# Kernel tuning notes

Hardware: AMD Instinct MI355X
Metric: run time of the kernel (lower is better)

Reference implementation:

```python
import jax, jax.numpy as jnp
import numpy as np

B, N, C = 64, 1024, 128


def setup_inputs() -> dict:
    key = jax.random.key(0)
    k1, k2, k3, k4, k5, k6 = jax.random.split(key, 6)
    adj_vals = jax.random.uniform(k1, (B, N, N), dtype=jnp.float32)
    mask = jax.random.uniform(k2, (B, N, N)) < 0.1
    adjacent = jnp.where(mask, adj_vals, 0.0)
    annotations = jax.random.normal(k3, (B, N, C), dtype=jnp.float32)
    # GraphConvolution bias, shape (1,1,C)
    gc_bias = jax.random.normal(k4, (1, 1, C), dtype=jnp.float32) * 0.05
    # Keras GRU params (reset_after=True default): kernel (C,3C), recurrent (C,3C), bias (2,3C)
    kernel = jax.random.normal(k5, (C, 3 * C), dtype=jnp.float32) / np.sqrt(C)
    recurrent_kernel = jax.random.normal(k6, (C, 3 * C), dtype=jnp.float32) / np.sqrt(C)
    gru_bias = jnp.zeros((2, 3 * C), dtype=jnp.float32)
    return {"adjacent": adjacent, "annotations": annotations, "gc_bias": gc_bias,
            "kernel": kernel, "recurrent_kernel": recurrent_kernel, "gru_bias": gru_bias}


def reference(adjacent, annotations, gc_bias, kernel, recurrent_kernel, gru_bias):
    # GraphConvolution: per-graph adj @ annotations, batched, + bias
    v = jnp.einsum('bij,bjc->bic', adjacent, annotations) + gc_bias  # [B,N,C]
    b, n, c = v.shape
    x = v.reshape(-1, c)            # visible states, one GRU step each
    h = annotations.reshape(-1, c)  # initial hidden states
    # single-step Keras GRU (reset_after=True)
    mx = x @ kernel + gru_bias[0]
    mh = h @ recurrent_kernel + gru_bias[1]
    xz, xr, xh = jnp.split(mx, 3, axis=-1)
    hz, hr, hh_in = jnp.split(mh, 3, axis=-1)
    z = jax.nn.sigmoid(xz + hz)
    r = jax.nn.sigmoid(xr + hr)
    hh = jnp.tanh(xh + r * hh_in)
    out = z * h + (1.0 - z) * hh
    return out.reshape(b, n, c)
```

## Files before the change

kernel.cpp:

```cpp
#include <hip/hip_runtime.h>

typedef unsigned short ushort_t;
typedef __attribute__((ext_vector_type(8))) short bf16x8;
typedef __attribute__((ext_vector_type(8))) unsigned short u16x8;
typedef __attribute__((ext_vector_type(4))) float f32x4;

#define B_ 64
#define N_ 1024
#define C_ 128

static __device__ __forceinline__ unsigned short f2bf(float f) {
  union { float f; unsigned int i; } v; v.f = f;
  unsigned int i = v.i;
  return (unsigned short)((i + 0x7FFFu + ((i >> 16) & 1u)) >> 16);
}
static __device__ __forceinline__ void split1(float x, ushort_t& h, ushort_t& l) {
  union { float f; unsigned int i; } u; u.f = x;
  h = (ushort_t)(u.i >> 16);
  union { unsigned int i; float f; } t; t.i = u.i & 0xFFFF0000u;
  union { float f; unsigned int i; } w; w.f = x - t.f;
  l = (ushort_t)(w.i >> 16);
}
static __device__ __forceinline__ bf16x8 as_bf(u16x8 v) {
  union { u16x8 u; bf16x8 b; } x; x.u = v; return x.b;
}
static __device__ __forceinline__ void gload_lds16(const void* g, void* l) {
  __builtin_amdgcn_global_load_lds((const __attribute__((address_space(1))) void*)g,
                                   (__attribute__((address_space(3))) void*)l,
                                   16, 0, 0);
}

__global__ __launch_bounds__(256) void tsplit(const float* __restrict__ src,
                                              ushort_t* __restrict__ dh,
                                              ushort_t* __restrict__ dl,
                                              int rows, int cols, long sb, long db) {
  __shared__ float tile[64][65];
  const int t = threadIdx.x;
  src += (long)blockIdx.z * sb;
  dh  += (long)blockIdx.z * db;
  dl  += (long)blockIdx.z * db;
  const int r0 = blockIdx.y * 64, c0 = blockIdx.x * 64;
#pragma unroll
  for (int p = 0; p < 4; ++p) {
    int row = p * 16 + (t >> 4), c4 = (t & 15) * 4;
    f32x4 v = *(const f32x4*)(src + (long)(r0 + row) * cols + c0 + c4);
#pragma unroll
    for (int j = 0; j < 4; ++j) tile[row][c4 + j] = v[j];
  }
  __syncthreads();
  const int oc = t >> 2;
#pragma unroll
  for (int p = 0; p < 2; ++p) {
    int ck = (t & 3) + p * 4;
    u16x8 vh, vl;
#pragma unroll
    for (int j = 0; j < 8; ++j) {
      ushort_t hj, lj;
      split1(tile[ck * 8 + j][oc], hj, lj);
      vh[j] = hj; vl[j] = lj;
    }
    long o = (long)(c0 + oc) * rows + r0 + ck * 8;
    *(u16x8*)(dh + o) = vh;
    *(u16x8*)(dl + o) = vl;
  }
}

__global__ __launch_bounds__(256, 2) void gc_gemm(const float* __restrict__ adj,
                                                  const ushort_t* __restrict__ annTh,
                                                  const ushort_t* __restrict__ annTl,
                                                  const float* __restrict__ gcb,
                                                  float* __restrict__ vout) {
  __shared__ __align__(16) ushort_t ldsAh[128 * 64];
  __shared__ __align__(16) ushort_t ldsAl[128 * 64];
  __shared__ __align__(16) ushort_t ldsBh[128 * 64];
  __shared__ __align__(16) ushort_t ldsBl[128 * 64];
  const int tid = threadIdx.x;
  const int w = tid >> 6, lane = tid & 63;
  const int wr = w >> 1, wc = w & 1;
  const int swz = (blockIdx.x & 7) * 64 + (blockIdx.x >> 3);
  const int b = swz >> 3;
  const int m0 = (swz & 7) * 128;

  const float*    adjb = adj   + ((long)b * N_ + m0) * N_;
  const ushort_t* aThb = annTh + (long)b * C_ * N_;
  const ushort_t* aTlb = annTl + (long)b * C_ * N_;

  const int srow8 = lane >> 3;
  const int klog  = ((lane & 7) * 16) ^ (srow8 << 4);
  const int fr = lane & 15;
  const int kg = lane >> 4;

  f32x4 acc[4][4] = {};

  for (int k0 = 0; k0 < N_; k0 += 64) {
#pragma unroll
    for (int jj = 0; jj < 4; ++jj) {
      int j = w * 4 + jj;
      long so = (long)(j * 8 + srow8) * N_ + k0 + (klog >> 1);
      gload_lds16(aThb + so, (void*)&ldsBh[j * 512]);
      gload_lds16(aTlb + so, (void*)&ldsBl[j * 512]);
    }
#pragma unroll
    for (int q = 0; q < 4; ++q) {
      int ch = q * 256 + tid;
      int row = ch >> 3, ce = ch & 7;
      const float* g = adjb + (long)row * N_ + k0 + ce * 8;
      f32x4 a0 = *(const f32x4*)g;
      f32x4 a1 = *(const f32x4*)(g + 4);
      u16x8 vh, vl;
#pragma unroll
      for (int j = 0; j < 4; ++j) {
        ushort_t hj, lj;
        split1(a0[j], hj, lj); vh[j] = hj; vl[j] = lj;
        split1(a1[j], hj, lj); vh[4 + j] = hj; vl[4 + j] = lj;
      }
      int kb = (ce * 16) ^ ((row & 7) << 4);
      *(u16x8*)((char*)ldsAh + row * 128 + kb) = vh;
      *(u16x8*)((char*)ldsAl + row * 128 + kb) = vl;
    }
    __syncthreads();
#pragma unroll
    for (int kk = 0; kk < 2; ++kk) {
      bf16x8 ah[4], al[4], bh[4], bl[4];
#pragma unroll
      for (int mi = 0; mi < 4; ++mi) {
        int row = wr * 64 + mi * 16 + fr;
        int kb = (kk * 64 + kg * 16) ^ ((row & 7) << 4);
        ah[mi] = *(const bf16x8*)((const char*)ldsAh + row * 128 + kb);
        al[mi] = *(const bf16x8*)((const char*)ldsAl + row * 128 + kb);
      }
#pragma unroll
      for (int ni = 0; ni < 4; ++ni) {
        int row = wc * 64 + ni * 16 + fr;
        int kb = (kk * 64 + kg * 16) ^ ((row & 7) << 4);
        bh[ni] = *(const bf16x8*)((const char*)ldsBh + row * 128 + kb);
        bl[ni] = *(const bf16x8*)((const char*)ldsBl + row * 128 + kb);
      }
#pragma unroll
      for (int mi = 0; mi < 4; ++mi)
#pragma unroll
        for (int ni = 0; ni < 4; ++ni) {
          acc[mi][ni] = __builtin_amdgcn_mfma_f32_16x16x32_bf16(ah[mi], bh[ni], acc[mi][ni], 0, 0, 0);
          acc[mi][ni] = __builtin_amdgcn_mfma_f32_16x16x32_bf16(al[mi], bh[ni], acc[mi][ni], 0, 0, 0);
          acc[mi][ni] = __builtin_amdgcn_mfma_f32_16x16x32_bf16(ah[mi], bl[ni], acc[mi][ni], 0, 0, 0);
        }
    }
    __syncthreads();
  }

  const long rowbase = (long)b * N_ + m0 + wr * 64;
#pragma unroll
  for (int ni = 0; ni < 4; ++ni) {
    int col = wc * 64 + ni * 16 + fr;
    float bias = gcb[col];
#pragma unroll
    for (int mi = 0; mi < 4; ++mi)
#pragma unroll
      for (int r = 0; r < 4; ++r)
        vout[(rowbase + mi * 16 + kg * 4 + r) * C_ + col] = acc[mi][ni][r] + bias;
  }
}

__global__ __launch_bounds__(256, 2) void gru(const float* __restrict__ v,
                                              const float* __restrict__ ann,
                                              const ushort_t* __restrict__ kTh,
                                              const ushort_t* __restrict__ kTl,
                                              const ushort_t* __restrict__ rTh,
                                              const float* __restrict__ gb,
                                              float* __restrict__ out) {
  const int w = threadIdx.x >> 6, lane = threadIdx.x & 63;
  const long m0 = ((long)blockIdx.x * 4 + w) * 32;
  const int fr = lane & 15, kg = lane >> 4;

  bf16x8 xh[2][4], xl[2][4], hh[2][4];
#pragma unroll
  for (int s = 0; s < 2; ++s)
#pragma unroll
    for (int kk = 0; kk < 4; ++kk) {
      long off = (m0 + s * 16 + fr) * (long)C_ + kk * 32 + kg * 8;
      f32x4 x0 = *(const f32x4*)(v + off);
      f32x4 x1 = *(const f32x4*)(v + off + 4);
      u16x8 th, tl;
#pragma unroll
      for (int j = 0; j < 4; ++j) {
        ushort_t hj, lj;
        split1(x0[j], hj, lj); th[j] = hj; tl[j] = lj;
        split1(x1[j], hj, lj); th[4 + j] = hj; tl[4 + j] = lj;
      }
      xh[s][kk] = as_bf(th); xl[s][kk] = as_bf(tl);
      f32x4 h0 = *(const f32x4*)(ann + off);
      f32x4 h1 = *(const f32x4*)(ann + off + 4);
      u16x8 hv;
#pragma unroll
      for (int j = 0; j < 4; ++j) { hv[j] = f2bf(h0[j]); hv[4 + j] = f2bf(h1[j]); }
      hh[s][kk] = as_bf(hv);
    }

  bf16x8 W0K[4], W0L[4], W0R[4], W1K[4], W1L[4], W1R[4];
  float HV0[8], HV1[8];

#define LOADW(WK, WL, WR, NN, GG)                                              \
  {                                                                            \
    const ushort_t* kh_ = kTh + (long)((GG) * C_ + (NN) * 16 + fr) * C_;       \
    const ushort_t* kl_ = kTl + (long)((GG) * C_ + (NN) * 16 + fr) * C_;       \
    const ushort_t* rh_ = rTh + (long)((GG) * C_ + (NN) * 16 + fr) * C_;       \
    _Pragma("unroll")                                                          \
    for (int kk = 0; kk < 4; ++kk) {                                           \
      int o_ = kk * 32 + kg * 8;                                               \
      WK[kk] = *(const bf16x8*)(kh_ + o_);                                     \
      WL[kk] = *(const bf16x8*)(kl_ + o_);                                     \
      WR[kk] = *(const bf16x8*)(rh_ + o_);                                     \
    }                                                                          \
  }

#define LOADHV(HV, NN)                                                         \
  _Pragma("unroll")                                                            \
  for (int s = 0; s < 2; ++s)                                                  \
    _Pragma("unroll")                                                          \
    for (int r = 0; r < 4; ++r)                                                \
      HV[s * 4 + r] = ann[(m0 + s * 16 + kg * 4 + r) * (long)C_ + (NN) * 16 + fr];

#define MATH(WK, WL, WR, AK0, AK1, AR0, AR1)                                   \
  {                                                                            \
    _Pragma("unroll")                                                          \
    for (int kk = 0; kk < 4; ++kk) {                                           \
      AK0 = __builtin_amdgcn_mfma_f32_16x16x32_bf16(xh[0][kk], WK[kk], AK0, 0, 0, 0); \
      AK1 = __builtin_amdgcn_mfma_f32_16x16x32_bf16(xh[1][kk], WK[kk], AK1, 0, 0, 0); \
      AK0 = __builtin_amdgcn_mfma_f32_16x16x32_bf16(xl[0][kk], WK[kk], AK0, 0, 0, 0); \
      AK1 = __builtin_amdgcn_mfma_f32_16x16x32_bf16(xl[1][kk], WK[kk], AK1, 0, 0, 0); \
      AK0 = __builtin_amdgcn_mfma_f32_16x16x32_bf16(xh[0][kk], WL[kk], AK0, 0, 0, 0); \
      AK1 = __builtin_amdgcn_mfma_f32_16x16x32_bf16(xh[1][kk], WL[kk], AK1, 0, 0, 0); \
    }                                                                          \
    _Pragma("unroll")                                                          \
    for (int kk = 0; kk < 4; ++kk) {                                           \
      AR0 = __builtin_amdgcn_mfma_f32_16x16x32_bf16(hh[0][kk], WR[kk], AR0, 0, 0, 0); \
      AR1 = __builtin_amdgcn_mfma_f32_16x16x32_bf16(hh[1][kk], WR[kk], AR1, 0, 0, 0); \
    }                                                                          \
  }

#define EPILOGUE(NN, HV)                                                       \
  {                                                                            \
    const int cb = (NN) * 16 + fr;                                             \
    const float bz  = gb[cb] + gb[384 + cb];                                   \
    const float brr = gb[128 + cb] + gb[384 + 128 + cb];                       \
    const float bxh = gb[256 + cb];                                            \
    const float bhi = gb[384 + 256 + cb];                                      \
    _Pragma("unroll")                                                          \
    for (int s = 0; s < 2; ++s) {                                              \
      const f32x4& az_ = s ? az1 : az0;                                        \
      const f32x4& ar_ = s ? ar1 : ar0;                                        \
      const f32x4& ax_ = s ? ax1 : ax0;                                        \
      const f32x4& ah_ = s ? ah1 : ah0;                                        \
      _Pragma("unroll")                                                        \
      for (int r = 0; r < 4; ++r) {                                            \
        long row = m0 + s * 16 + kg * 4 + r;                                   \
        float hval = HV[s * 4 + r];                                            \
        float zz = 1.f / (1.f + __expf(-(az_[r] + bz)));                       \
        float rr = 1.f / (1.f + __expf(-(ar_[r] + brr)));                      \
        float hpre = ax_[r] + bxh + rr * (ah_[r] + bhi);                       \
        hpre = fminf(fmaxf(hpre, -15.f), 15.f);                                \
        float e2 = __expf(2.f * hpre);                                         \
        float th = (e2 - 1.f) / (e2 + 1.f);                                    \
        out[row * C_ + cb] = zz * hval + (1.f - zz) * th;                      \
      }                                                                        \
    }                                                                          \
  }

  LOADW(W0K, W0L, W0R, 0, 0)
  LOADHV(HV0, 0)

#pragma unroll 1
  for (int n = 0; n < 8; n += 2) {
    {
      f32x4 az0 = {}, az1 = {}, ar0 = {}, ar1 = {}, ax0 = {}, ax1 = {}, ah0 = {}, ah1 = {};
      LOADW(W1K, W1L, W1R, n, 1)
      MATH(W0K, W0L, W0R, az0, az1, az0, az1)
      LOADW(W0K, W0L, W0R, n, 2)
      MATH(W1K, W1L, W1R, ar0, ar1, ar0, ar1)
      LOADW(W1K, W1L, W1R, n + 1, 0)
      LOADHV(HV1, n + 1)
      MATH(W0K, W0L, W0R, ax0, ax1, ah0, ah1)
      EPILOGUE(n, HV0)
    }
    {
      f32x4 az0 = {}, az1 = {}, ar0 = {}, ar1 = {}, ax0 = {}, ax1 = {}, ah0 = {}, ah1 = {};
      LOADW(W0K, W0L, W0R, n + 1, 1)
      MATH(W1K, W1L, W1R, az0, az1, az0, az1)
      LOADW(W1K, W1L, W1R, n + 1, 2)
      MATH(W0K, W0L, W0R, ar0, ar1, ar0, ar1)
      const int nn2 = (n + 2 < 8) ? (n + 2) : 0;
      LOADW(W0K, W0L, W0R, nn2, 0)
      LOADHV(HV0, nn2)
      MATH(W1K, W1L, W1R, ax0, ax1, ah0, ah1)
      EPILOGUE(n + 1, HV1)
    }
  }
#undef LOADW
#undef LOADHV
#undef MATH
#undef EPILOGUE
}

extern "C" void kernel_launch(void* const* d_in, const int* in_sizes, int n_in,
                              void* d_out, int out_size, void* d_ws, size_t ws_size,
                              hipStream_t stream) {
  const float* adj = (const float*)d_in[0];
  const float* ann = (const float*)d_in[1];
  const float* gcb = (const float*)d_in[2];
  const float* ker = (const float*)d_in[3];
  const float* rk  = (const float*)d_in[4];
  const float* gb  = (const float*)d_in[5];
  float* out = (float*)d_out;

  char* ws = (char*)d_ws;
  ushort_t* annTh = (ushort_t*)(ws);
  ushort_t* annTl = (ushort_t*)(ws + 16777216);
  ushort_t* kTh   = (ushort_t*)(ws + 33554432);
  ushort_t* kTl   = (ushort_t*)(ws + 33652736);
  ushort_t* rTh   = (ushort_t*)(ws + 33751040);
  ushort_t* rTl   = (ushort_t*)(ws + 33849344);
  float*    vbuf  = (float*)(ws + 33947648);

  hipLaunchKernelGGL(tsplit, dim3(2, 16, 64), dim3(256), 0, stream,
                     ann, annTh, annTl, 1024, 128, (long)1024 * 128, (long)128 * 1024);
  hipLaunchKernelGGL(tsplit, dim3(6, 2, 1), dim3(256), 0, stream,
                     ker, kTh, kTl, 128, 384, 0L, 0L);
  hipLaunchKernelGGL(tsplit, dim3(6, 2, 1), dim3(256), 0, stream,
                     rk, rTh, rTl, 128, 384, 0L, 0L);
  hipLaunchKernelGGL(gc_gemm, dim3(512), dim3(256), 0, stream,
                     adj, annTh, annTl, gcb, vbuf);
  hipLaunchKernelGGL(gru, dim3(512), dim3(256), 0, stream,
                     vbuf, ann, kTh, kTl, rTh, gb, out);
}
```

Baseline: 203.6 us.

## Double-buffer gc_gemm with direct fp32 adjacency loads to LDS and in-register split

Reworks the adjacency GEMM main loop so the fp32 adjacency tile is copied straight into LDS with async global-to-LDS loads, instead of being loaded into registers, split into bf16 hi/lo and written to LDS. The bf16 split now happens after the LDS read, just before the MFMAs. LDS is double-buffered with a K-step of 32, so the next tile's loads are issued while the current tile is computed, with one barrier per iteration. The aim is to hide global memory latency and drop the register-staged conversion path. In exchange each wave repeats the split work in its compute phase and runs twice as many loop iterations.

```diff
diff --git a/kernel.cpp b/kernel.cpp
--- a/kernel.cpp
+++ b/kernel.cpp
@@ -70,10 +70,9 @@
                                                   const ushort_t* __restrict__ annTl,
                                                   const float* __restrict__ gcb,
                                                   float* __restrict__ vout) {
-  __shared__ __align__(16) ushort_t ldsAh[128 * 64];
-  __shared__ __align__(16) ushort_t ldsAl[128 * 64];
-  __shared__ __align__(16) ushort_t ldsBh[128 * 64];
-  __shared__ __align__(16) ushort_t ldsBl[128 * 64];
+  __shared__ __align__(16) float    ldsA [2 * 4096];
+  __shared__ __align__(16) ushort_t ldsBh[2 * 4096];
+  __shared__ __align__(16) ushort_t ldsBl[2 * 4096];
   const int tid = threadIdx.x;
   const int w = tid >> 6, lane = tid & 63;
   const int wr = w >> 1, wc = w & 1;
@@ -85,68 +84,84 @@
   const ushort_t* aThb = annTh + (long)b * C_ * N_;
   const ushort_t* aTlb = annTl + (long)b * C_ * N_;
 
-  const int srow8 = lane >> 3;
-  const int klog  = ((lane & 7) * 16) ^ (srow8 << 4);
   const int fr = lane & 15;
   const int kg = lane >> 4;
 
+  const int aRow  = lane >> 3;
+  const int aCs   = (lane & 7) ^ aRow;
+  const int bRow  = lane >> 2;
+  const int bCs   = (lane & 3) ^ ((lane >> 3) & 3);
+
   f32x4 acc[4][4] = {};
 
-  for (int k0 = 0; k0 < N_; k0 += 64) {
-#pragma unroll
-    for (int jj = 0; jj < 4; ++jj) {
-      int j = w * 4 + jj;
-      long so = (long)(j * 8 + srow8) * N_ + k0 + (klog >> 1);
-      gload_lds16(aThb + so, (void*)&ldsBh[j * 512]);
-      gload_lds16(aTlb + so, (void*)&ldsBl[j * 512]);
-    }
-#pragma unroll
-    for (int q = 0; q < 4; ++q) {
-      int ch = q * 256 + tid;
-      int row = ch >> 3, ce = ch & 7;
-      const float* g = adjb + (long)row * N_ + k0 + ce * 8;
-      f32x4 a0 = *(const f32x4*)g;
-      f32x4 a1 = *(const f32x4*)(g + 4);
-      u16x8 vh, vl;
-#pragma unroll
-      for (int j = 0; j < 4; ++j) {
-        ushort_t hj, lj;
-        split1(a0[j], hj, lj); vh[j] = hj; vl[j] = lj;
-        split1(a1[j], hj, lj); vh[4 + j] = hj; vl[4 + j] = lj;
-      }
-      int kb = (ce * 16) ^ ((row & 7) << 4);
-      *(u16x8*)((char*)ldsAh + row * 128 + kb) = vh;
-      *(u16x8*)((char*)ldsAl + row * 128 + kb) = vl;
-    }
+#define STAGE(CUR, T)                                                          \
+  {                                                                            \
+    const int k0_ = (T) * 32;                                                  \
+    _Pragma("unroll")                                                          \
+    for (int jj = 0; jj < 4; ++jj) {                                           \
+      int j_ = w * 4 + jj;                                                     \
+      gload_lds16(adjb + (long)(j_ * 8 + aRow) * N_ + k0_ + aCs * 4,           \
+                  (void*)(ldsA + (CUR) * 4096 + j_ * 256));                    \
+    }                                                                          \
+    _Pragma("unroll")                                                          \
+    for (int jj = 0; jj < 2; ++jj) {                                           \
+      int j_ = w * 2 + jj;                                                     \
+      long so_ = (long)(j_ * 16 + bRow) * N_ + k0_ + bCs * 8;                  \
+      gload_lds16(aThb + so_, (void*)(ldsBh + (CUR) * 4096 + j_ * 512));       \
+      gload_lds16(aTlb + so_, (void*)(ldsBl + (CUR) * 4096 + j_ * 512));       \
+    }                                                                          \
+  }
+
+#define COMPUTE(CUR)                                                           \
+  {                                                                            \
+    bf16x8 bh_[4], bl_[4], ah_[4], al_[4];                                     \
+    _Pragma("unroll")                                                          \
+    for (int ni = 0; ni < 4; ++ni) {                                           \
+      int row_ = wc * 64 + ni * 16 + fr;                                       \
+      int kb_ = (kg << 4) ^ ((((row_) >> 1) & 3) << 4);                        \
+      const char* base_ = (const char*)(ldsBh + (CUR) * 4096) + row_ * 64 + kb_; \
+      const char* basl_ = (const char*)(ldsBl + (CUR) * 4096) + row_ * 64 + kb_; \
+      bh_[ni] = *(const bf16x8*)base_;                                         \
+      bl_[ni] = *(const bf16x8*)basl_;                                         \
+    }                                                                          \
+    _Pragma("unroll")                                                          \
+    for (int mi = 0; mi < 4; ++mi) {                                           \
+      int row_ = wr * 64 + mi * 16 + fr;                                       \
+      int b0_ = row_ * 128 + ((kg * 32) ^ ((row_ & 7) << 4));                  \
+      f32x4 a0_ = *(const f32x4*)((const char*)(ldsA + (CUR) * 4096) + b0_);   \
+      f32x4 a1_ = *(const f32x4*)((const char*)(ldsA + (CUR) * 4096) + (b0_ ^ 16)); \
+      u16x8 vh_, vl_;                                                          \
+      _Pragma("unroll")                                                        \
+      for (int j = 0; j < 4; ++j) {                                            \
+        ushort_t hj_, lj_;                                                     \
+        split1(a0_[j], hj_, lj_); vh_[j] = hj_;     vl_[j] = lj_;              \
+        split1(a1_[j], hj_, lj_); vh_[4 + j] = hj_; vl_[4 + j] = lj_;          \
+      }                                                                        \
+      ah_[mi] = as_bf(vh_); al_[mi] = as_bf(vl_);                              \
+    }                                                                          \
+    _Pragma("unroll")                                                          \
+    for (int mi = 0; mi < 4; ++mi)                                             \
+      _Pragma("unroll")                                                        \
+      for (int ni = 0; ni < 4; ++ni) {                                         \
+        acc[mi][ni] = __builtin_amdgcn_mfma_f32_16x16x32_bf16(ah_[mi], bh_[ni], acc[mi][ni], 0, 0, 0); \
+        acc[mi][ni] = __builtin_amdgcn_mfma_f32_16x16x32_bf16(al_[mi], bh_[ni], acc[mi][ni], 0, 0, 0); \
+        acc[mi][ni] = __builtin_amdgcn_mfma_f32_16x16x32_bf16(ah_[mi], bl_[ni], acc[mi][ni], 0, 0, 0); \
+      }                                                                        \
+  }
+
+  STAGE(0, 0)
+  __syncthreads();
+
+#pragma unroll 1
+  for (int t = 0; t < 32; ++t) {
+    const int cur = t & 1;
+    if (t < 31) { STAGE(cur ^ 1, t + 1) }
+    COMPUTE(cur)
     __syncthreads();
-#pragma unroll
-    for (int kk = 0; kk < 2; ++kk) {
-      bf16x8 ah[4], al[4], bh[4], bl[4];
-#pragma unroll
-      for (int mi = 0; mi < 4; ++mi) {
-        int row = wr * 64 + mi * 16 + fr;
-        int kb = (kk * 64 + kg * 16) ^ ((row & 7) << 4);
-        ah[mi] = *(const bf16x8*)((const char*)ldsAh + row * 128 + kb);
-        al[mi] = *(const bf16x8*)((const char*)ldsAl + row * 128 + kb);
-      }
-#pragma unroll
-      for (int ni = 0; ni < 4; ++ni) {
-        int row = wc * 64 + ni * 16 + fr;
-        int kb = (kk * 64 + kg * 16) ^ ((row & 7) << 4);
-        bh[ni] = *(const bf16x8*)((const char*)ldsBh + row * 128 + kb);
-        bl[ni] = *(const bf16x8*)((const char*)ldsBl + row * 128 + kb);
-      }
-#pragma unroll
-      for (int mi = 0; mi < 4; ++mi)
-#pragma unroll
-        for (int ni = 0; ni < 4; ++ni) {
-          acc[mi][ni] = __builtin_amdgcn_mfma_f32_16x16x32_bf16(ah[mi], bh[ni], acc[mi][ni], 0, 0, 0);
-          acc[mi][ni] = __builtin_amdgcn_mfma_f32_16x16x32_bf16(al[mi], bh[ni], acc[mi][ni], 0, 0, 0);
-          acc[mi][ni] = __builtin_amdgcn_mfma_f32_16x16x32_bf16(ah[mi], bl[ni], acc[mi][ni], 0, 0, 0);
-        }
-    }
-    __syncthreads();
-  }
+  }
+
+#undef STAGE
+#undef COMPUTE
 
   const long rowbase = (long)b * N_ + m0 + wr * 64;
 #pragma unroll
```

Measured after the change: 206.4 us. Within noise of the previous version (+1.3%).
